# Performance work log

Hardware: AMD Instinct MI355X
Metric: run time of the kernel (lower is better)

The kernel has to match this reference:

```python
import math
import jax, jax.numpy as jnp
import numpy as np

EMB = 1024
NHEADS = 16
CTX = 2048
LN_EPS = 1e-5


def new_gelu(x):
    c = math.sqrt(2.0 / math.pi)
    return 0.5 * x * (1.0 + jnp.tanh(c * (x + 0.044715 * x * x * x)))


def layer_norm(x, g, b):
    mu = jnp.mean(x, axis=-1, keepdims=True)
    var = jnp.mean(jnp.square(x - mu), axis=-1, keepdims=True)
    return (x - mu) * jax.lax.rsqrt(var + LN_EPS) * g + b


def setup_inputs() -> dict:
    key = jax.random.key(0)
    ks = jax.random.split(key, 12)
    s = 0.02
    return {
        "x": jax.random.normal(ks[0], (2, 2048, EMB), dtype=jnp.float32),
        "ln1_g": jnp.ones((EMB,), jnp.float32),
        "ln1_b": jnp.zeros((EMB,), jnp.float32),
        "W_attn": jax.random.normal(ks[1], (EMB, 3 * EMB), jnp.float32) * s,
        "b_attn": jnp.zeros((3 * EMB,), jnp.float32),
        "W_attn_proj": jax.random.normal(ks[2], (EMB, EMB), jnp.float32) * s,
        "b_attn_proj": jnp.zeros((EMB,), jnp.float32),
        "ln2_g": jnp.ones((EMB,), jnp.float32),
        "ln2_b": jnp.zeros((EMB,), jnp.float32),
        "W_fc": jax.random.normal(ks[3], (EMB, 4 * EMB), jnp.float32) * s,
        "b_fc": jnp.zeros((4 * EMB,), jnp.float32),
        "W_mlp_proj": jax.random.normal(ks[4], (4 * EMB, EMB), jnp.float32) * s,
        "b_mlp_proj": jnp.zeros((EMB,), jnp.float32),
    }


def reference(x, ln1_g, ln1_b, W_attn, b_attn, W_attn_proj, b_attn_proj,
              ln2_g, ln2_b, W_fc, b_fc, W_mlp_proj, b_mlp_proj):
    B, S, E = x.shape
    hd = E // NHEADS

    # x = ln_1(x)
    x = layer_norm(x, ln1_g, ln1_b)

    # attention on normalized x
    qkv = x @ W_attn + b_attn                      # [B,S,3E]
    q, k, v = jnp.split(qkv, 3, axis=-1)
    q = q.reshape(B, S, NHEADS, hd).transpose(0, 2, 1, 3)  # [B,H,S,hd]
    k = k.reshape(B, S, NHEADS, hd).transpose(0, 2, 1, 3)
    v = v.reshape(B, S, NHEADS, hd).transpose(0, 2, 1, 3)

    attn = jnp.einsum("bhqd,bhkd->bhqk", q, k) * (1.0 / math.sqrt(hd))
    causal = jnp.tril(jnp.ones((S, S), dtype=bool))
    attn = jnp.where(causal[None, None], attn, -jnp.inf)
    attn = jax.nn.softmax(attn, axis=-1)
    out = jnp.einsum("bhqk,bhkd->bhqd", attn, v)   # [B,H,S,hd]
    out = out.transpose(0, 2, 1, 3).reshape(B, S, E)
    out = out @ W_attn_proj + b_attn_proj

    x = x + out

    # x = ln_2(x)
    x = layer_norm(x, ln2_g, ln2_b)

    # MLP on normalized x
    h = new_gelu(x @ W_fc + b_fc)
    h = h @ W_mlp_proj + b_mlp_proj
    return x + h
```

## Files before the change

kernel.cpp:

```cpp
#include <hip/hip_runtime.h>
#include <cstdint>

typedef __attribute__((ext_vector_type(8))) short bf16x8;
typedef __attribute__((ext_vector_type(4))) float f32x4;
typedef __attribute__((ext_vector_type(16))) float f32x16;
typedef __attribute__((ext_vector_type(4))) unsigned short u16x4;
typedef __attribute__((ext_vector_type(4))) unsigned int u32x4;
typedef unsigned short u16;

#define LOG2E 1.44269504088896340736f

__device__ __forceinline__ u16 f2bf(float f) {
  unsigned u = __builtin_bit_cast(unsigned, f);
  u += 0x7FFFu + ((u >> 16) & 1u);
  return (u16)(u >> 16);
}
__device__ __forceinline__ float bf2f(u16 h) {
  return __builtin_bit_cast(float, ((unsigned)h) << 16);
}

#define GLOAD_LDS16(g, l)                                                              \
  __builtin_amdgcn_global_load_lds((const __attribute__((address_space(1))) void*)(g), \
                                   (__attribute__((address_space(3))) void*)(l), 16, 0, 0)

__global__ __launch_bounds__(256) void k_transpose_all(
    const float* __restrict__ W0, u16* __restrict__ T0,
    const float* __restrict__ W1, u16* __restrict__ T1,
    const float* __restrict__ W2, u16* __restrict__ T2,
    const float* __restrict__ W3, u16* __restrict__ T3) {
  __shared__ float tile[32][33];
  int b = blockIdx.x;
  const float* W;
  u16* Wt;
  int K, N, nx;
  if (b < 3072)        { W = W0; Wt = T0; K = 1024; N = 3072; nx = 96; }
  else if (b < 4096)   { b -= 3072; W = W1; Wt = T1; K = 1024; N = 1024; nx = 32; }
  else if (b < 8192)   { b -= 4096; W = W2; Wt = T2; K = 1024; N = 4096; nx = 128; }
  else                 { b -= 8192; W = W3; Wt = T3; K = 4096; N = 1024; nx = 32; }
  const int n0 = (b % nx) * 32, k0 = (b / nx) * 32;
  const int tid = threadIdx.x;
  const int tx = tid & 31, ty = tid >> 5;
#pragma unroll
  for (int i = 0; i < 32; i += 8)
    tile[ty + i][tx] = W[(size_t)(k0 + ty + i) * N + n0 + tx];
  __syncthreads();
#pragma unroll
  for (int i = 0; i < 32; i += 8)
    Wt[(size_t)(n0 + ty + i) * K + k0 + tx] = f2bf(tile[tx][ty + i]);
}

template <bool INF32>
__global__ __launch_bounds__(256) void k_layernorm(
    const void* __restrict__ xin, const float* __restrict__ g,
    const float* __restrict__ b, u16* __restrict__ y) {
  const int row = blockIdx.x, tid = threadIdx.x;
  float v0, v1, v2, v3;
  if (INF32) {
    const float4 v = ((const float4*)((const float*)xin + (size_t)row * 1024))[tid];
    v0 = v.x; v1 = v.y; v2 = v.z; v3 = v.w;
  } else {
    const u16x4 v = ((const u16x4*)((const u16*)xin + (size_t)row * 1024))[tid];
    v0 = bf2f(v[0]); v1 = bf2f(v[1]); v2 = bf2f(v[2]); v3 = bf2f(v[3]);
  }
  float s = v0 + v1 + v2 + v3;
#pragma unroll
  for (int m = 1; m < 64; m <<= 1) s += __shfl_xor(s, m);
  __shared__ float ps[8];
  if ((tid & 63) == 0) ps[tid >> 6] = s;
  __syncthreads();
  const float mean = (ps[0] + ps[1] + ps[2] + ps[3]) * (1.0f / 1024.0f);
  const float d0 = v0 - mean, d1 = v1 - mean, d2 = v2 - mean, d3 = v3 - mean;
  float s2 = d0 * d0 + d1 * d1 + d2 * d2 + d3 * d3;
#pragma unroll
  for (int m = 1; m < 64; m <<= 1) s2 += __shfl_xor(s2, m);
  if ((tid & 63) == 0) ps[4 + (tid >> 6)] = s2;
  __syncthreads();
  const float var = (ps[4] + ps[5] + ps[6] + ps[7]) * (1.0f / 1024.0f);
  const float rstd = rsqrtf(var + 1e-5f);
  const float4 gv = ((const float4*)g)[tid];
  const float4 bv = ((const float4*)b)[tid];
  u16x4 o;
  o[0] = f2bf(d0 * rstd * gv.x + bv.x);
  o[1] = f2bf(d1 * rstd * gv.y + bv.y);
  o[2] = f2bf(d2 * rstd * gv.z + bv.z);
  o[3] = f2bf(d3 * rstd * gv.w + bv.w);
  *(u16x4*)(y + (size_t)row * 1024 + tid * 4) = o;
}

__device__ __forceinline__ float gelu_f(float x) {
  const float u = 0.7978845608028654f * (x + 0.044715f * x * x * x);
  const float e = exp2f(u * 2.8853900817779268f);
  const float t = 1.0f - 2.0f / (e + 1.0f);
  return 0.5f * x * (1.0f + t);
}

template <int EPI, int BN>
__global__ __launch_bounds__(256, 4) void k_gemm_bt(
    const u16* __restrict__ A, const u16* __restrict__ Bt,
    const float* __restrict__ bias, const u16* __restrict__ resid,
    void* __restrict__ out, u16* __restrict__ vt, int M, int N, int K, int nbx) {
  constexpr int BM = 128;
  __shared__ u16 As[BM * 64];
  __shared__ u16 Bs[BN * 64];
  const int tid = threadIdx.x;
  const int wg = ((blockIdx.x & 7) * (gridDim.x >> 3)) + (blockIdx.x >> 3);
  const int bx = wg % nbx, by = wg / nbx;
  const int rowBase = by * BM, colBase = bx * BN;
  const int w = tid >> 6, l = tid & 63;
  const int wm = (BN == 128) ? (w >> 1) : w;
  const int wn = (BN == 128) ? (w & 1) : 0;
  constexpr int MR = (BN == 128) ? 4 : 2;
  constexpr int WROWS = (BN == 128) ? 64 : 32;
  const int lrow = l & 15, lg = l >> 4;
  const int srow = tid >> 3, sslot = tid & 7;

  const f32x4 fz = {0.f, 0.f, 0.f, 0.f};
  f32x4 acc[MR][4];
#pragma unroll
  for (int m = 0; m < MR; m++)
#pragma unroll
    for (int n = 0; n < 4; n++) acc[m][n] = fz;

  const int NT = K >> 6;
  for (int kt = 0; kt < NT; ++kt) {
#pragma unroll
    for (int i = 0; i < BM / 32; i++) {
      const int r = srow + 32 * i;
      const int gs = sslot ^ (r & 7);
      GLOAD_LDS16(A + (size_t)(rowBase + r) * K + kt * 64 + gs * 8,
                  (char*)As + i * 4096 + tid * 16);
    }
#pragma unroll
    for (int i = 0; i < BN / 32; i++) {
      const int r = srow + 32 * i;
      const int gs = sslot ^ (r & 7);
      GLOAD_LDS16(Bt + (size_t)(colBase + r) * K + kt * 64 + gs * 8,
                  (char*)Bs + i * 4096 + tid * 16);
    }
    __syncthreads();
#pragma unroll
    for (int kc = 0; kc < 2; kc++) {
      bf16x8 av[MR], bv[4];
#pragma unroll
      for (int m = 0; m < MR; m++) {
        const int r = wm * WROWS + m * 16 + lrow;
        const int sl = (kc * 4 + lg) ^ (r & 7);
        av[m] = *(const bf16x8*)((const char*)As + r * 128 + sl * 16);
      }
#pragma unroll
      for (int n = 0; n < 4; n++) {
        const int r = wn * 64 + n * 16 + lrow;
        const int sl = (kc * 4 + lg) ^ (r & 7);
        bv[n] = *(const bf16x8*)((const char*)Bs + r * 128 + sl * 16);
      }
#pragma unroll
      for (int m = 0; m < MR; m++)
#pragma unroll
        for (int n = 0; n < 4; n++)
          acc[m][n] = __builtin_amdgcn_mfma_f32_16x16x32_bf16(av[m], bv[n], acc[m][n], 0, 0, 0);
    }
    __syncthreads();
  }
#pragma unroll
  for (int n = 0; n < 4; n++) {
    const int col = colBase + wn * 64 + n * 16 + lrow;
    const float bval = bias[col];
#pragma unroll
    for (int m = 0; m < MR; m++) {
      const int row0 = rowBase + wm * WROWS + m * 16 + lg * 4;
      if (EPI == 3 && col >= 2048) {
        const int c2 = col - 2048;
        const int hh = c2 >> 6, dd = c2 & 63;
        const int bat = row0 >> 11, tok0 = row0 & 2047;
        u16x4 pk;
#pragma unroll
        for (int r = 0; r < 4; r++) pk[r] = f2bf(acc[m][n][r] + bval);
        *(u16x4*)(vt + ((size_t)(bat * 16 + hh) * 64 + dd) * 2048 + tok0) = pk;
      } else if (EPI == 3) {
#pragma unroll
        for (int r = 0; r < 4; r++)
          ((u16*)out)[(size_t)(row0 + r) * 2048 + col] = f2bf(acc[m][n][r] + bval);
      } else {
#pragma unroll
        for (int r = 0; r < 4; r++) {
          const size_t idx = (size_t)(row0 + r) * N + col;
          float v = acc[m][n][r] + bval;
          if (EPI == 0) {
            ((u16*)out)[idx] = f2bf(v);
          } else if (EPI == 2) {
            ((u16*)out)[idx] = f2bf(gelu_f(v));
          } else if (EPI == 4) {
            ((u16*)out)[idx] = f2bf(v + bf2f(resid[idx]));
          } else {
            v += bf2f(resid[idx]);
            ((float*)out)[idx] = v;
          }
        }
      }
    }
  }
}

__global__ __launch_bounds__(256, 2) void k_attention(
    const u16* __restrict__ qk, const u16* __restrict__ VT, u16* __restrict__ out) {
  const int S = 2048, E2 = 2048;
  const int bid = blockIdx.x;
  const int qt = 15 - (bid >> 5);
  const int bh = bid & 31;
  const int bat = bh >> 4, h = bh & 15;
  const u16* base = qk + (size_t)bat * S * E2;
  const u16* kbase = base + 1024 + h * 64;
  const u16* vbase = VT + (size_t)bh * 64 * S;
  const int tid = threadIdx.x, w = tid >> 6, l = tid & 63;
  const int l31 = l & 31, lh = l >> 5;
  __shared__ u16 Ks[2][64 * 64];
  __shared__ u16 Vs[2][64 * 64];
  const int srow = tid >> 3;
  const int gs = (tid & 7) ^ (srow & 7);
  const float sc = 0.125f * LOG2E;
  const float RTHR = 8.0f / sc;

  auto STAGE = [&](int bufi, int kb) {
#pragma unroll
    for (int round = 0; round < 2; round++) {
      const int r = srow + 32 * round;
      GLOAD_LDS16(kbase + (size_t)(kb + r) * E2 + gs * 8, (char*)Ks[bufi] + round * 4096 + tid * 16);
      GLOAD_LDS16(vbase + (size_t)r * S + kb + gs * 8, (char*)Vs[bufi] + round * 4096 + tid * 16);
    }
  };

  const int wq0 = qt * 128 + w * 32;
  const int qg = wq0 + l31;
  const int tdiag = wq0 >> 6;
  const int nkt = 2 * qt + 2;

  bf16x8 qf[4];
#pragma unroll
  for (int s = 0; s < 4; s++)
    qf[s] = *(const bf16x8*)(base + (size_t)qg * E2 + h * 64 + s * 16 + lh * 8);

  f32x16 o0, o1;
#pragma unroll
  for (int r = 0; r < 16; r++) { o0[r] = 0.f; o1[r] = 0.f; }
  float mrow = -1e30f, lsum = 0.f;

  STAGE(0, 0);
  __syncthreads();

  for (int t = 0; t < nkt; t++) {
    const int cur = t & 1;
    const int kb = t * 64;
    if (t + 1 < nkt) STAGE(cur ^ 1, kb + 64);
    if (t <= tdiag) {
      const u16* Kc = Ks[cur];
      const u16* Vc = Vs[cur];

      f32x16 sv0, sv1;
#pragma unroll
      for (int r = 0; r < 16; r++) { sv0[r] = 0.f; sv1[r] = 0.f; }
#pragma unroll
      for (int s = 0; s < 4; s++) {
        const int row0 = l31, row1 = 32 + l31;
        const int sl = s * 2 + lh;
        const bf16x8 k0 = *(const bf16x8*)(Kc + row0 * 64 + ((sl ^ (row0 & 7)) * 8));
        const bf16x8 k1 = *(const bf16x8*)(Kc + row1 * 64 + ((sl ^ (row1 & 7)) * 8));
        sv0 = __builtin_amdgcn_mfma_f32_32x32x16_bf16(k0, qf[s], sv0, 0, 0, 0);
        sv1 = __builtin_amdgcn_mfma_f32_32x32x16_bf16(k1, qf[s], sv1, 0, 0, 0);
      }

      if (t == tdiag) {
#pragma unroll
        for (int reg = 0; reg < 16; reg++) {
          const int kl = (reg & 3) + 8 * (reg >> 2) + 4 * lh;
          if (kb + kl > qg) sv0[reg] = -1e30f;
          if (kb + 32 + kl > qg) sv1[reg] = -1e30f;
        }
      }

      float tmax = sv0[0];
#pragma unroll
      for (int reg = 1; reg < 16; reg++) tmax = fmaxf(tmax, sv0[reg]);
#pragma unroll
      for (int reg = 0; reg < 16; reg++) tmax = fmaxf(tmax, sv1[reg]);
      tmax = fmaxf(tmax, __shfl_xor(tmax, 32));

      if (!__all(tmax - mrow <= RTHR)) {
        const float mnew = fmaxf(mrow, tmax);
        const float corr = exp2f((mrow - mnew) * sc);
        lsum *= corr;
#pragma unroll
        for (int reg = 0; reg < 16; reg++) { o0[reg] *= corr; o1[reg] *= corr; }
        mrow = mnew;
      }
      const float msc = mrow * sc;

      float p0[16], p1[16];
      float rsum = 0.f;
#pragma unroll
      for (int reg = 0; reg < 16; reg++) {
        p0[reg] = exp2f(fmaf(sv0[reg], sc, -msc));
        p1[reg] = exp2f(fmaf(sv1[reg], sc, -msc));
        rsum += p0[reg] + p1[reg];
      }
      rsum += __shfl_xor(rsum, 32);
      lsum += rsum;

      unsigned pk0[8], pk1[8], ex0[8], ex1[8];
#pragma unroll
      for (int j = 0; j < 8; j++) {
        asm("v_cvt_pk_bf16_f32 %0, %1, %2" : "=v"(pk0[j]) : "v"(p0[2 * j]), "v"(p0[2 * j + 1]));
        asm("v_cvt_pk_bf16_f32 %0, %1, %2" : "=v"(pk1[j]) : "v"(p1[2 * j]), "v"(p1[2 * j + 1]));
        ex0[j] = (unsigned)__shfl_xor((int)pk0[j], 32);
        ex1[j] = (unsigned)__shfl_xor((int)pk1[j], 32);
      }
      const bool lo = (lh == 0);

#pragma unroll
      for (int kh = 0; kh < 2; kh++) {
#pragma unroll
        for (int sl2 = 0; sl2 < 2; sl2++) {
          const int ks = kh * 2 + sl2;
          const unsigned* pk = kh ? pk1 : pk0;
          const unsigned* ex = kh ? ex1 : ex0;
          const int j0 = sl2 * 4;
          const unsigned b0 = lo ? pk[j0 + 0] : ex[j0 + 2];
          const unsigned b1 = lo ? pk[j0 + 1] : ex[j0 + 3];
          const unsigned b2 = lo ? ex[j0 + 0] : pk[j0 + 2];
          const unsigned b3 = lo ? ex[j0 + 1] : pk[j0 + 3];
          const u32x4 pbu = {b0, b1, b2, b3};
          const bf16x8 pb = __builtin_bit_cast(bf16x8, pbu);
          const int sl = ks * 2 + lh;
          const int r0 = l31, r1 = 32 + l31;
          const bf16x8 v0 = *(const bf16x8*)(Vc + r0 * 64 + ((sl ^ (r0 & 7)) * 8));
          const bf16x8 v1 = *(const bf16x8*)(Vc + r1 * 64 + ((sl ^ (r1 & 7)) * 8));
          o0 = __builtin_amdgcn_mfma_f32_32x32x16_bf16(v0, pb, o0, 0, 0, 0);
          o1 = __builtin_amdgcn_mfma_f32_32x32x16_bf16(v1, pb, o1, 0, 0, 0);
        }
      }
    }
    __syncthreads();
  }

  const float inv = 1.0f / lsum;
  const size_t orow = (size_t)(bat * S + qg) * 1024 + h * 64;
#pragma unroll
  for (int g = 0; g < 4; g++) {
    u16x4 s0, s1;
#pragma unroll
    for (int r = 0; r < 4; r++) {
      s0[r] = f2bf(o0[4 * g + r] * inv);
      s1[r] = f2bf(o1[4 * g + r] * inv);
    }
    const int d0 = 8 * g + 4 * lh;
    *(u16x4*)(out + orow + d0) = s0;
    *(u16x4*)(out + orow + 32 + d0) = s1;
  }
}

extern "C" void kernel_launch(void* const* d_in, const int* in_sizes, int n_in,
                              void* d_out, int out_size, void* d_ws, size_t ws_size,
                              hipStream_t stream) {
  (void)in_sizes; (void)n_in; (void)out_size; (void)ws_size;
  const float* x      = (const float*)d_in[0];
  const float* ln1_g  = (const float*)d_in[1];
  const float* ln1_b  = (const float*)d_in[2];
  const float* W_attn = (const float*)d_in[3];
  const float* b_attn = (const float*)d_in[4];
  const float* W_proj = (const float*)d_in[5];
  const float* b_proj = (const float*)d_in[6];
  const float* ln2_g  = (const float*)d_in[7];
  const float* ln2_b  = (const float*)d_in[8];
  const float* W_fc   = (const float*)d_in[9];
  const float* b_fc   = (const float*)d_in[10];
  const float* W_mlp  = (const float*)d_in[11];
  const float* b_mlp  = (const float*)d_in[12];

  const int M = 4096;
  char* ws = (char*)d_ws;
  size_t off = 0;
  auto alloc = [&](size_t bytes) {
    void* p = ws + off;
    off += (bytes + 255) & ~(size_t)255;
    return p;
  };
  u16* WattnT = (u16*)alloc((size_t)3072 * 1024 * 2);
  u16* WprojT = (u16*)alloc((size_t)1024 * 1024 * 2);
  u16* WfcT   = (u16*)alloc((size_t)4096 * 1024 * 2);
  u16* WmlpT  = (u16*)alloc((size_t)1024 * 4096 * 2);
  u16* x1     = (u16*)alloc((size_t)M * 1024 * 2);
  u16* qkb    = (u16*)alloc((size_t)M * 2048 * 2);
  u16* VT     = (u16*)alloc((size_t)32 * 64 * 2048 * 2);
  u16* attno  = (u16*)alloc((size_t)M * 1024 * 2);
  u16* x2     = (u16*)alloc((size_t)M * 1024 * 2);
  u16* x3     = (u16*)alloc((size_t)M * 1024 * 2);
  u16* hbuf   = (u16*)alloc((size_t)M * 4096 * 2);

  const dim3 blk(256);
  k_transpose_all<<<dim3(12288), blk, 0, stream>>>(
      W_attn, WattnT, W_proj, WprojT, W_fc, WfcT, W_mlp, WmlpT);

  k_layernorm<true><<<M, blk, 0, stream>>>(x, ln1_g, ln1_b, x1);
  k_gemm_bt<3, 128><<<dim3(768), blk, 0, stream>>>(
      x1, WattnT, b_attn, nullptr, qkb, VT, M, 3072, 1024, 24);
  k_attention<<<dim3(512), blk, 0, stream>>>(qkb, VT, attno);
  k_gemm_bt<4, 64><<<dim3(512), blk, 0, stream>>>(
      attno, WprojT, b_proj, x1, x2, nullptr, M, 1024, 1024, 16);
  k_layernorm<false><<<M, blk, 0, stream>>>(x2, ln2_g, ln2_b, x3);
  k_gemm_bt<2, 128><<<dim3(1024), blk, 0, stream>>>(
      x3, WfcT, b_fc, nullptr, hbuf, nullptr, M, 4096, 1024, 32);
  k_gemm_bt<1, 64><<<dim3(512), blk, 0, stream>>>(
      hbuf, WmlpT, b_mlp, x3, d_out, nullptr, M, 1024, 4096, 16);
}
```

Before: 244.6 us.

## Stage GEMM epilogue through LDS for coalesced 16-byte global stores

The GEMM epilogue now writes bias-added (and GELU'd) results into a padded shared-memory tile, then reads them back row-contiguously so each thread issues 16-byte vector stores, including the transposed V output and the residual-add paths. This replaces scattered 2-byte and 4-byte column-strided stores that use global write bandwidth poorly. It adds LDS traffic and extra barriers, enlarges the shared allocation (which may reduce occupancy), and for the bf16 residual path it now rounds to bf16 before adding the residual, which slightly changes numerics.

```diff
diff --git a/kernel.cpp b/kernel.cpp
--- a/kernel.cpp
+++ b/kernel.cpp
@@ -100,8 +100,13 @@
     const float* __restrict__ bias, const u16* __restrict__ resid,
     void* __restrict__ out, u16* __restrict__ vt, int M, int N, int K, int nbx) {
   constexpr int BM = 128;
-  __shared__ u16 As[BM * 64];
-  __shared__ u16 Bs[BN * 64];
+  constexpr int LOOPB = (BM * 64 + BN * 64) * 2;
+  constexpr int STP = BN + 8;
+  constexpr int EPIB = (EPI == 1) ? 64 * 68 * 4 : BM * STP * 2;
+  constexpr int SMB = LOOPB > EPIB ? LOOPB : EPIB;
+  __shared__ char smem[SMB];
+  u16* As = (u16*)smem;
+  u16* Bs = (u16*)(smem + BM * 64 * 2);
   const int tid = threadIdx.x;
   const int wg = ((blockIdx.x & 7) * (gridDim.x >> 3)) + (blockIdx.x >> 3);
   const int bx = wg % nbx, by = wg / nbx;
@@ -161,41 +166,86 @@
     }
     __syncthreads();
   }
-#pragma unroll
-  for (int n = 0; n < 4; n++) {
-    const int col = colBase + wn * 64 + n * 16 + lrow;
-    const float bval = bias[col];
+
+  if (EPI == 1) {
+    float* stgf = (float*)smem;
 #pragma unroll
     for (int m = 0; m < MR; m++) {
-      const int row0 = rowBase + wm * WROWS + m * 16 + lg * 4;
-      if (EPI == 3 && col >= 2048) {
-        const int c2 = col - 2048;
-        const int hh = c2 >> 6, dd = c2 & 63;
-        const int bat = row0 >> 11, tok0 = row0 & 2047;
-        u16x4 pk;
-#pragma unroll
-        for (int r = 0; r < 4; r++) pk[r] = f2bf(acc[m][n][r] + bval);
-        *(u16x4*)(vt + ((size_t)(bat * 16 + hh) * 64 + dd) * 2048 + tok0) = pk;
-      } else if (EPI == 3) {
-#pragma unroll
-        for (int r = 0; r < 4; r++)
-          ((u16*)out)[(size_t)(row0 + r) * 2048 + col] = f2bf(acc[m][n][r] + bval);
-      } else {
+      if (m) __syncthreads();
+#pragma unroll
+      for (int n = 0; n < 4; n++) {
+        const int col = n * 16 + lrow;
+        const float bval = bias[colBase + col];
+        const int pr0 = wm * 16 + lg * 4;
+#pragma unroll
+        for (int r = 0; r < 4; r++) stgf[(pr0 + r) * 68 + col] = acc[m][n][r] + bval;
+      }
+      __syncthreads();
+#pragma unroll
+      for (int i = 0; i < 4; i++) {
+        const int c = i * 256 + tid;
+        const int pr = c >> 4, ch = c & 15;
+        float4 d = *(float4*)(stgf + pr * 68 + ch * 4);
+        const int grow = rowBase + ((pr >> 4) << 5) + m * 16 + (pr & 15);
+        const size_t gidx = (size_t)grow * N + colBase + ch * 4;
+        const u16x4 rr = *(const u16x4*)(resid + gidx);
+        d.x += bf2f(rr[0]); d.y += bf2f(rr[1]); d.z += bf2f(rr[2]); d.w += bf2f(rr[3]);
+        *(float4*)((float*)out + gidx) = d;
+      }
+    }
+  } else {
+    u16* stg = (u16*)smem;
+    const bool vpath = (EPI == 3) && (colBase >= 2048);
+#pragma unroll
+    for (int n = 0; n < 4; n++) {
+      const int col = wn * 64 + n * 16 + lrow;
+      const float bval = bias[colBase + col];
+#pragma unroll
+      for (int m = 0; m < MR; m++) {
+        const int lr0 = wm * WROWS + m * 16 + lg * 4;
 #pragma unroll
         for (int r = 0; r < 4; r++) {
-          const size_t idx = (size_t)(row0 + r) * N + col;
           float v = acc[m][n][r] + bval;
-          if (EPI == 0) {
-            ((u16*)out)[idx] = f2bf(v);
-          } else if (EPI == 2) {
-            ((u16*)out)[idx] = f2bf(gelu_f(v));
-          } else if (EPI == 4) {
-            ((u16*)out)[idx] = f2bf(v + bf2f(resid[idx]));
-          } else {
-            v += bf2f(resid[idx]);
-            ((float*)out)[idx] = v;
+          if (EPI == 2) v = gelu_f(v);
+          if (vpath)
+            stg[col * STP + lr0 + r] = f2bf(v);
+          else
+            stg[(lr0 + r) * STP + col] = f2bf(v);
+        }
+      }
+    }
+    __syncthreads();
+    if (vpath) {
+      const int cb = colBase - 2048;
+      const int bat = rowBase >> 11, tok0 = rowBase & 2047;
+#pragma unroll
+      for (int i = 0; i < 8; i++) {
+        const int c = i * 256 + tid;
+        const int cr = c >> 4, ch = c & 15;
+        const u32x4 d = *(u32x4*)(stg + cr * STP + ch * 8);
+        const int hh = (cb + cr) >> 6, dd = (cb + cr) & 63;
+        *(u32x4*)(vt + ((size_t)(bat * 16 + hh) * 64 + dd) * 2048 + tok0 + ch * 8) = d;
+      }
+    } else {
+      const int outN = (EPI == 3) ? 2048 : N;
+      constexpr int CH = BN / 8;
+#pragma unroll
+      for (int i = 0; i < BM * CH / 256; i++) {
+        const int c = i * 256 + tid;
+        const int row = c / CH, ch = c % CH;
+        u32x4 d = *(u32x4*)(stg + row * STP + ch * 8);
+        const size_t gidx = (size_t)(rowBase + row) * outN + colBase + ch * 8;
+        if (EPI == 4) {
+          const u32x4 rr = *(const u32x4*)(resid + gidx);
+#pragma unroll
+          for (int j = 0; j < 4; j++) {
+            const unsigned a = d[j], b = rr[j];
+            const unsigned lo2 = (unsigned)f2bf(bf2f((u16)a) + bf2f((u16)b));
+            const unsigned hi2 = (unsigned)f2bf(bf2f((u16)(a >> 16)) + bf2f((u16)(b >> 16)));
+            d[j] = lo2 | (hi2 << 16);
           }
         }
+        *(u32x4*)((u16*)out + gidx) = d;
       }
     }
   }
```

Measured after the change: 245.6 us. About the same (+0.4%).
